# Kernel optimization log

Measured on AMD Instinct MI355X. Metric: run time of the kernel, lower is better.

Reference implementation:

```python
import jax, jax.numpy as jnp
import numpy as np

HIDDEN = 2048
NUM_V = 16
NUM_K = 8
HK = 128
HV = 128
KCONV = 4
KEY_DIM = NUM_K * HK      # 1024
VALUE_DIM = NUM_V * HV    # 2048
CONV_DIM = 2 * KEY_DIM + VALUE_DIM  # 4096
R = NUM_V // NUM_K        # 2
L2_EPS = 1e-6
NORM_EPS = 1e-6


def setup_inputs() -> dict:
    key = jax.random.key(0)
    ks = jax.random.split(key, 8)
    s = 0.02
    return {
        "hidden_states": jax.random.normal(ks[0], (1, 1024, HIDDEN), jnp.float32),
        "w_qkvz": jax.random.normal(ks[1], (2 * KEY_DIM + 2 * VALUE_DIM, HIDDEN), jnp.float32) * s,
        "w_ba": jax.random.normal(ks[2], (2 * NUM_V, HIDDEN), jnp.float32) * s,
        "conv_w": jax.random.normal(ks[3], (CONV_DIM, KCONV), jnp.float32) * s,
        "dt_bias": jnp.ones((NUM_V,), jnp.float32),
        "A_log": jnp.log(jax.random.uniform(ks[4], (NUM_V,), jnp.float32, 1e-3, 16.0)),
        "norm_weight": jnp.ones((HV,), jnp.float32),
        "w_out": jax.random.normal(ks[5], (HIDDEN, VALUE_DIM), jnp.float32) * s,
    }


def reference(hidden_states, w_qkvz, w_ba, conv_w, dt_bias, A_log, norm_weight, w_out):
    B, T, _ = hidden_states.shape
    # --- input projections ---
    qkvz = hidden_states @ w_qkvz.T                     # [B,T,2K+2V]
    ba = hidden_states @ w_ba.T                         # [B,T,2*Hv]
    # fix_query_key_value_ordering: group by k-head, layout [hk, hk, r*hv, r*hv]
    qkvz = qkvz.reshape(B, T, NUM_K, 2 * HK + 2 * R * HV)
    q, k, v, z = jnp.split(qkvz, [HK, 2 * HK, 2 * HK + R * HV], axis=3)
    v = v.reshape(B, T, NUM_V, HV)
    z = z.reshape(B, T, NUM_V, HV)
    ba = ba.reshape(B, T, NUM_K, 2 * R)
    b = ba[..., :R].reshape(B, T, NUM_V)
    a = ba[..., R:].reshape(B, T, NUM_V)
    # --- depthwise causal conv1d + silu over concatenated q,k,v ---
    mixed = jnp.concatenate(
        [q.reshape(B, T, KEY_DIM), k.reshape(B, T, KEY_DIM), v.reshape(B, T, VALUE_DIM)], axis=-1
    )
    xc = mixed.transpose(0, 2, 1)                       # [B,C,T]
    yc = jax.lax.conv_general_dilated(
        xc, conv_w[:, None, :], (1,), [(KCONV - 1, 0)],
        feature_group_count=CONV_DIM, dimension_numbers=("NCH", "OIH", "NCH"),
    )
    yc = jax.nn.silu(yc).transpose(0, 2, 1)             # [B,T,C]
    q, k, v = jnp.split(yc, [KEY_DIM, 2 * KEY_DIM], axis=-1)
    q = q.reshape(B, T, NUM_K, HK)
    k = k.reshape(B, T, NUM_K, HK)
    v = v.reshape(B, T, NUM_V, HV)
    # --- gates ---
    beta = jax.nn.sigmoid(b)                            # [B,T,Hv]
    g = -jnp.exp(A_log) * jax.nn.softplus(a + dt_bias)  # [B,T,Hv] (log decay, <=0)
    # GQA expansion of q,k to value heads
    q = jnp.repeat(q, R, axis=2)                        # [B,T,Hv,hk]
    k = jnp.repeat(k, R, axis=2)
    # l2 norm on q,k (use_qk_l2norm_in_kernel=True)
    q = q * jax.lax.rsqrt(jnp.sum(q * q, -1, keepdims=True) + L2_EPS)
    k = k * jax.lax.rsqrt(jnp.sum(k * k, -1, keepdims=True) + L2_EPS)
    scale = HK ** -0.5
    # --- gated delta rule recurrence ---
    def step(S, xs):
        qt, kt, vt, gt, bt = xs                          # per-timestep slices
        S = S * jnp.exp(gt)[..., None, None]             # decay state [B,Hv,hk,hv]
        kv = jnp.einsum("bhk,bhkv->bhv", kt, S)          # readout at k_t
        delta = (vt - kv) * bt[..., None]                # beta-gated delta
        S = S + jnp.einsum("bhk,bhv->bhkv", kt, delta)
        o = jnp.einsum("bhk,bhkv->bhv", qt * scale, S)
        return S, o

    S0 = jnp.zeros((B, NUM_V, HK, HV), hidden_states.dtype)
    xs = (
        q.transpose(1, 0, 2, 3), k.transpose(1, 0, 2, 3), v.transpose(1, 0, 2, 3),
        g.transpose(1, 0, 2), beta.transpose(1, 0, 2),
    )
    _, o = jax.lax.scan(step, S0, xs)                   # o: [T,B,Hv,hv]
    o = o.transpose(1, 0, 2, 3)                         # [B,T,Hv,hv]
    # --- gated RMSNorm (gate applied before normalization, Mamba2/Qwen3Next style) ---
    xf = o.astype(jnp.float32) * jax.nn.silu(z.astype(jnp.float32))
    var = jnp.mean(xf * xf, -1, keepdims=True)
    xn = xf * jax.lax.rsqrt(var + NORM_EPS) * norm_weight
    # --- output projection ---
    return xn.reshape(B, T, VALUE_DIM) @ w_out.T
```

## Files before the change

### kernel.cpp

```cpp
#include <hip/hip_runtime.h>
#include <math.h>

#define T_LEN   1024
#define HIDDEN  2048
#define QKVZ_N  6144
#define VAL_DIM 2048

typedef _Float16 half8 __attribute__((ext_vector_type(8)));
typedef _Float16 half4 __attribute__((ext_vector_type(4)));
typedef _Float16 half2t __attribute__((ext_vector_type(2)));
typedef float floatx4 __attribute__((ext_vector_type(4)));

__device__ __forceinline__ float sigmoidf_(float x) { return 1.f / (1.f + expf(-x)); }

__device__ __forceinline__ void gl_lds16(const _Float16* g, _Float16* l) {
    __builtin_amdgcn_global_load_lds(
        (const __attribute__((address_space(1))) void*)g,
        (__attribute__((address_space(3))) void*)l, 16, 0, 0);
}

__global__ __launch_bounds__(256) void cvt3(const float* __restrict__ s0, _Float16* __restrict__ d0, int n0,
                                            const float* __restrict__ s1, _Float16* __restrict__ d1, int n1,
                                            const float* __restrict__ s2, _Float16* __restrict__ d2, int n2) {
    int i = blockIdx.x * 256 + threadIdx.x;
    const float* s;
    _Float16* d;
    if (i < n0) { s = s0; d = d0; }
    else if (i < n0 + n1) { s = s1; d = d1; i -= n0; }
    else if (i < n0 + n1 + n2) { s = s2; d = d2; i -= n0 + n1; }
    else return;
    const float4 v = ((const float4*)s)[i];
    half4 h;
    h[0] = (_Float16)v.x; h[1] = (_Float16)v.y;
    h[2] = (_Float16)v.z; h[3] = (_Float16)v.w;
    *(half4*)&d[i * 4] = h;
}

template <int NT, typename OutT>
__global__ __launch_bounds__(256, 2) void gemm_h16(const _Float16* __restrict__ A,
                                                   const _Float16* __restrict__ W,
                                                   OutT* __restrict__ C,
                                                   int MB, int NB, int K) {
    const int BN = NT * 32;
    const int N = NB * BN;
    const int l = blockIdx.x;
    const int x = l & 7;
    const int tt = l >> 3;
    const int mb = tt % MB;
    const int nb = x + 8 * (tt / MB);
    const int m0 = mb * 64, n0 = nb * BN;

    const int t = threadIdx.x;
    const int wave = t >> 6;
    const int lane = t & 63;
    const int wr = (wave >> 1) * 32;
    const int wc = (wave & 1) * (BN / 2);
    const int l15 = lane & 15;
    const int quad = lane >> 4;
    const int srow = lane >> 3;
    const int slot = lane & 7;

    __shared__ __align__(16) _Float16 Ah[2][4096];
    __shared__ __align__(16) _Float16 Bh[2][BN * 64];

    floatx4 acc[2][NT];
#pragma unroll
    for (int i = 0; i < 2; ++i)
#pragma unroll
        for (int j = 0; j < NT; ++j) acc[i][j] = 0;

    auto stage = [&](int buf, int k0) {
#pragma unroll
        for (int g = 0; g < 2; ++g) {
            const int r = wave * 16 + g * 8 + srow;
            const int kc = slot ^ (r & 7);
            gl_lds16(A + (size_t)(m0 + r) * K + k0 + kc * 8,
                     &Ah[buf][(wave * 128 + g * 64) * 8]);
        }
#pragma unroll
        for (int g = 0; g < NT; ++g) {
            const int r = wave * (NT * 8) + g * 8 + srow;
            const int kc = slot ^ (r & 7);
            gl_lds16(W + (size_t)(n0 + r) * K + k0 + kc * 8,
                     &Bh[buf][(wave * (NT * 64) + g * 64) * 8]);
        }
    };

    const int NIT = K >> 6;
    stage(0, 0);
    __syncthreads();
    int cur = 0;
    for (int it = 0; it < NIT; ++it) {
        if (it + 1 < NIT) stage(cur ^ 1, (it + 1) * 64);
        half8 af[2][2], bf[NT][2];
#pragma unroll
        for (int mt = 0; mt < 2; ++mt)
#pragma unroll
            for (int ks = 0; ks < 2; ++ks) {
                const int m = wr + mt * 16 + l15;
                const int kq = ks * 4 + quad;
                af[mt][ks] = *(const half8*)&Ah[cur][(m * 8 + (kq ^ (m & 7))) * 8];
            }
#pragma unroll
        for (int nt = 0; nt < NT; ++nt)
#pragma unroll
            for (int ks = 0; ks < 2; ++ks) {
                const int n = wc + nt * 16 + l15;
                const int kq = ks * 4 + quad;
                bf[nt][ks] = *(const half8*)&Bh[cur][(n * 8 + (kq ^ (n & 7))) * 8];
            }
#pragma unroll
        for (int mt = 0; mt < 2; ++mt)
#pragma unroll
            for (int nt = 0; nt < NT; ++nt)
#pragma unroll
                for (int ks = 0; ks < 2; ++ks)
                    acc[mt][nt] = __builtin_amdgcn_mfma_f32_16x16x32_f16(
                        af[mt][ks], bf[nt][ks], acc[mt][nt], 0, 0, 0);
        if (it + 1 < NIT) {
            __syncthreads();
            cur ^= 1;
        }
    }
#pragma unroll
    for (int mt = 0; mt < 2; ++mt)
#pragma unroll
        for (int nt = 0; nt < NT; ++nt) {
            const int c = n0 + wc + nt * 16 + l15;
#pragma unroll
            for (int reg = 0; reg < 4; ++reg) {
                const int r = m0 + wr + mt * 16 + quad * 4 + reg;
                C[(size_t)r * N + c] = (OutT)acc[mt][nt][reg];
            }
        }
}

__global__ __launch_bounds__(256) void gemm_ba_gates(const float* __restrict__ A,
                                                     const float* __restrict__ W,
                                                     const float* __restrict__ dt_bias,
                                                     const float* __restrict__ A_log,
                                                     float* __restrict__ lgd,
                                                     float* __restrict__ bet) {
    const int m = blockIdx.x;
    const int tid = threadIdx.x;
    const int kl = tid & 31;
    const int ng = tid >> 5;
    const float* Arow = A + (size_t)m * 2048;
    __shared__ float sba[32];

    float4 a4[16];
#pragma unroll
    for (int j = 0; j < 16; ++j)
        a4[j] = *(const float4*)(Arow + j * 128 + kl * 4);

#pragma unroll
    for (int nn = 0; nn < 4; ++nn) {
        const int n = nn * 8 + ng;
        const float* Wrow = W + (size_t)n * 2048;
        float acc = 0.f;
#pragma unroll
        for (int j = 0; j < 16; ++j) {
            const float4 w4 = *(const float4*)(Wrow + j * 128 + kl * 4);
            acc = fmaf(a4[j].x, w4.x, acc);
            acc = fmaf(a4[j].y, w4.y, acc);
            acc = fmaf(a4[j].z, w4.z, acc);
            acc = fmaf(a4[j].w, w4.w, acc);
        }
        acc += __shfl_xor(acc, 1, 64);
        acc += __shfl_xor(acc, 2, 64);
        acc += __shfl_xor(acc, 4, 64);
        acc += __shfl_xor(acc, 8, 64);
        acc += __shfl_xor(acc, 16, 64);
        if (kl == 0) sba[n] = acc;
    }
    __syncthreads();
    if (tid < 16) {
        const int vh = tid, kh = vh >> 1, r = vh & 1;
        const float b = sba[kh * 4 + r];
        const float a = sba[kh * 4 + 2 + r];
        bet[m * 16 + vh] = 1.f / (1.f + expf(-b));
        const float xx = a + dt_bias[vh];
        const float sp = (xx > 0.f) ? (xx + log1pf(expf(-xx))) : log1pf(expf(xx));
        lgd[m * 16 + vh] = -expf(A_log[vh]) * sp;
    }
}

__global__ __launch_bounds__(512) void conv_silu_l2(const _Float16* __restrict__ qkvz,
                                                    const float* __restrict__ conv_w,
                                                    _Float16* __restrict__ qc,
                                                    _Float16* __restrict__ kc,
                                                    _Float16* __restrict__ vc) {
    const int t = blockIdx.x;
    const int c = threadIdx.x * 8;
    int col;
    _Float16* dst;
    bool isqk;
    float extra = 1.f;
    if (c < 1024) {
        col = ((c >> 7) * 768) + (c & 127);
        dst = qc + t * 1024 + c;
        isqk = true;
        extra = 0.08838834764831845f;
    } else if (c < 2048) {
        const int cc = c - 1024;
        col = ((cc >> 7) * 768) + 128 + (cc & 127);
        dst = kc + t * 1024 + cc;
        isqk = true;
    } else {
        const int cc = c - 2048;
        col = ((cc >> 8) * 768) + 256 + (cc & 255);
        dst = vc + (size_t)t * 2048 + cc;
        isqk = false;
    }
    const size_t gb = (size_t)t * QKVZ_N + col;
    const half8 x3 = *(const half8*)(qkvz + gb);
    half8 x2, x1, x0;
    if (t >= 1) x2 = *(const half8*)(qkvz + gb - QKVZ_N);
    if (t >= 2) x1 = *(const half8*)(qkvz + gb - 2 * (size_t)QKVZ_N);
    if (t >= 3) x0 = *(const half8*)(qkvz + gb - 3 * (size_t)QKVZ_N);

    float y[8];
    float ss = 0.f;
#pragma unroll
    for (int u = 0; u < 8; ++u) {
        const float4 wv = *(const float4*)(conv_w + (c + u) * 4);
        float acc = (float)x3[u] * wv.w;
        if (t >= 1) acc = fmaf((float)x2[u], wv.z, acc);
        if (t >= 2) acc = fmaf((float)x1[u], wv.y, acc);
        if (t >= 3) acc = fmaf((float)x0[u], wv.x, acc);
        acc = acc * (1.f / (1.f + expf(-acc)));
        y[u] = acc;
        ss = fmaf(acc, acc, ss);
    }
    half8 ov;
    if (isqk) {
        ss += __shfl_xor(ss, 1, 64);
        ss += __shfl_xor(ss, 2, 64);
        ss += __shfl_xor(ss, 4, 64);
        ss += __shfl_xor(ss, 8, 64);
        const float r = rsqrtf(ss + 1e-6f) * extra;
#pragma unroll
        for (int u = 0; u < 8; ++u) ov[u] = (_Float16)(y[u] * r);
    } else {
#pragma unroll
        for (int u = 0; u < 8; ++u) ov[u] = (_Float16)y[u];
    }
    *(half8*)dst = ov;
}

__global__ __launch_bounds__(256, 1) void chunk_prep(
    const _Float16* __restrict__ qch, const _Float16* __restrict__ kch,
    const _Float16* __restrict__ vch, const float* __restrict__ lgd,
    const float* __restrict__ bet, _Float16* __restrict__ CH,
    float* __restrict__ gamC) {
    const int blk = blockIdx.x;
    const int c = blk >> 4, h = blk & 15, kh = h >> 1;
    const int c0 = c * 64;
    const int tid = threadIdx.x, lane = tid & 63, wave = tid >> 6;
    const int l15 = lane & 15, quad = lane >> 4;

    __shared__ __align__(16) _Float16 Ksh[8192];
    __shared__ __align__(16) _Float16 Qsh[8192];
    __shared__ __align__(16) float Amat[64 * 68];
    __shared__ float Gs[64], Bets[64], Gam[64];

#pragma unroll
    for (int i = 0; i < 17; ++i) Amat[tid + i * 256] = 0.f;

    {
        const int t = tid >> 2, kc0 = (tid & 3) * 4;
        const size_t gb = (size_t)(c0 + t) * 1024 + kh * 128;
#pragma unroll
        for (int i = 0; i < 4; ++i) {
            const int kc = kc0 + i;
            half8 kv = *(const half8*)(kch + gb + kc * 8);
            half8 qv = *(const half8*)(qch + gb + kc * 8);
            const int chl = t * 16 + (kc ^ (t & 15));
            *(half8*)&Ksh[chl * 8] = kv;
            *(half8*)&Qsh[chl * 8] = qv;
        }
    }
    if (tid < 64) {
        float g = lgd[(size_t)(c0 + tid) * 16 + h];
#pragma unroll
        for (int off = 1; off < 64; off <<= 1) {
            float y = __shfl_up(g, off, 64);
            if (tid >= off) g += y;
        }
        Gs[tid] = g;
        Gam[tid] = expf(g);
        Bets[tid] = bet[(size_t)(c0 + tid) * 16 + h];
    }
    __syncthreads();

    _Float16* CHb = CH + (size_t)(c * 16 + h) * 36864;
    _Float16* Ug = CHb;
    _Float16* Wtg = CHb + 8192;
    _Float16* Khg = CHb + 16384;
    _Float16* Qgg = CHb + 24576;
    _Float16* Lg = CHb + 32768;

    {
        floatx4 accKK[4], accQK[4];
#pragma unroll
        for (int tt = 0; tt < 4; ++tt) { accKK[tt] = 0; accQK[tt] = 0; }
        half8 bfK[4];
#pragma unroll
        for (int ks = 0; ks < 4; ++ks) {
            const int i = wave * 16 + l15;
            const int kc = ks * 4 + quad;
            bfK[ks] = *(const half8*)&Ksh[(i * 16 + (kc ^ (i & 15))) * 8];
        }
#pragma unroll
        for (int tt = 0; tt < 4; ++tt) {
            const int t = tt * 16 + l15;
#pragma unroll
            for (int ks = 0; ks < 4; ++ks) {
                const int kc = ks * 4 + quad;
                const int chl = (t * 16 + (kc ^ (t & 15))) * 8;
                half8 afK = *(const half8*)&Ksh[chl];
                half8 afQ = *(const half8*)&Qsh[chl];
                accKK[tt] = __builtin_amdgcn_mfma_f32_16x16x32_f16(afK, bfK[ks], accKK[tt], 0, 0, 0);
                accQK[tt] = __builtin_amdgcn_mfma_f32_16x16x32_f16(afQ, bfK[ks], accQK[tt], 0, 0, 0);
            }
        }
        const int ii = wave * 16 + l15;
        const float Gi = Gs[ii];
#pragma unroll
        for (int tt = 0; tt < 4; ++tt)
#pragma unroll
            for (int r = 0; r < 4; ++r) {
                const int t = tt * 16 + quad * 4 + r;
                const float Gt = Gs[t];
                const float ratio = (ii <= t) ? expf(Gt - Gi) : 0.f;
                if (ii < t) Amat[t * 68 + ii] = Bets[t] * ratio * accKK[tt][r];
                Lg[t * 64 + ii] = (_Float16)((ii <= t) ? ratio * accQK[tt][r] : 0.f);
            }
    }
    __syncthreads();

    {
        const int j = tid;
        float x[64];
        if (j < 128) {
#pragma unroll
            for (int t = 0; t < 64; ++t)
                x[t] = Bets[t] * (float)vch[(size_t)(c0 + t) * 2048 + h * 128 + j];
        } else {
            const int k = j - 128;
#pragma unroll
            for (int t = 0; t < 64; ++t) {
                const int chl = t * 16 + ((k >> 3) ^ (t & 15));
                x[t] = Bets[t] * Gam[t] * (float)Ksh[chl * 8 + (k & 7)];
            }
        }
#pragma unroll
        for (int t = 1; t < 64; ++t) {
            const int nq = (t + 3) >> 2;
            float s0 = 0.f, s1 = 0.f, s2 = 0.f, s3 = 0.f;
#pragma unroll
            for (int q = 0; q < nq; ++q) {
                const float4 a = *(const float4*)&Amat[t * 68 + q * 4];
                s0 = fmaf(a.x, x[q * 4 + 0], s0);
                s1 = fmaf(a.y, x[q * 4 + 1], s1);
                s2 = fmaf(a.z, x[q * 4 + 2], s2);
                s3 = fmaf(a.w, x[q * 4 + 3], s3);
            }
            x[t] -= (s0 + s1) + (s2 + s3);
        }
        if (j < 128) {
#pragma unroll
            for (int t = 0; t < 64; t += 4) {
                half4 w4;
                w4[0] = (_Float16)x[t]; w4[1] = (_Float16)x[t + 1];
                w4[2] = (_Float16)x[t + 2]; w4[3] = (_Float16)x[t + 3];
                *(half4*)&Wtg[j * 64 + t] = w4;
            }
        } else {
            const int k = j - 128;
#pragma unroll
            for (int t = 0; t < 64; ++t) Ug[t * 128 + k] = (_Float16)x[t];
        }
    }

    {
        const float g63 = Gs[63];
        const int k = tid >> 1, cb = (tid & 1) * 32;
#pragma unroll
        for (int cc = 0; cc < 32; cc += 4) {
            half4 o4;
#pragma unroll
            for (int u = 0; u < 4; ++u) {
                const int ci = cb + cc + u;
                const int chl = ci * 16 + ((k >> 3) ^ (ci & 15));
                o4[u] = (_Float16)(expf(g63 - Gs[ci]) * (float)Ksh[chl * 8 + (k & 7)]);
            }
            *(half4*)&Khg[k * 64 + cb + cc] = o4;
        }
        const int cq = tid >> 2, kb = (tid & 3) * 4;
        const float gam = Gam[cq];
#pragma unroll
        for (int kc = 0; kc < 4; ++kc) {
            const int kcc = kb + kc;
            half8 q8 = *(const half8*)&Qsh[(cq * 16 + (kcc ^ (cq & 15))) * 8];
            half8 s8;
#pragma unroll
            for (int u = 0; u < 8; ++u) s8[u] = (_Float16)(gam * (float)q8[u]);
            *(half8*)&Qgg[cq * 128 + kcc * 8] = s8;
        }
        if (tid == 0) gamC[c * 16 + h] = Gam[63];
    }
}

struct ScanOps {
    half8 aU[4];
    half8 aQ[4];
    half8 aL[2];
    half8 aK[2][2];
    half4 wv;
    float gC;
};

__global__ __launch_bounds__(256) void chunk_scan(const _Float16* __restrict__ CH,
                                                  const float* __restrict__ gamC,
                                                  float* __restrict__ o) {
    const int h = blockIdx.x & 15;
    const int vsl = blockIdx.x >> 4;
    const int tid = threadIdx.x, lane = tid & 63, wave = tid >> 6;
    const int l15 = lane & 15, quad = lane >> 4;
    const int tw = wave * 16;
    const int kw = wave * 32;
    const int sKey = l15 << 1;
    const int dKey = (l15 << 1) & 14;

    __shared__ __align__(16) _Float16 Ssh[16 * 128];
    __shared__ __align__(16) _Float16 Dsh[16 * 64];

    *(half8*)&Ssh[tid * 8] = half8{0, 0, 0, 0, 0, 0, 0, 0};
    floatx4 Sacc[2];
    Sacc[0] = 0; Sacc[1] = 0;
    __syncthreads();

    auto loadOps = [&](ScanOps& S, int c) {
        const _Float16* CHb = CH + (size_t)(c * 16 + h) * 36864;
#pragma unroll
        for (int ks = 0; ks < 4; ++ks) {
            S.aU[ks] = *(const half8*)(CHb + (tw + l15) * 128 + ks * 32 + quad * 8);
            S.aQ[ks] = *(const half8*)(CHb + 24576 + (tw + l15) * 128 + ks * 32 + quad * 8);
        }
#pragma unroll
        for (int cs = 0; cs < 2; ++cs) {
            S.aL[cs] = *(const half8*)(CHb + 32768 + (tw + l15) * 64 + cs * 32 + quad * 8);
#pragma unroll
            for (int kt = 0; kt < 2; ++kt)
                S.aK[kt][cs] = *(const half8*)(CHb + 16384 + (kw + kt * 16 + l15) * 64 + cs * 32 + quad * 8);
        }
        S.wv = *(const half4*)(CHb + 8192 + (vsl * 16 + l15) * 64 + tw + quad * 4);
        S.gC = gamC[c * 16 + h];
    };

    auto chunkBody = [&](const ScanOps& S, int c) {
        half8 bs[4];
#pragma unroll
        for (int ks = 0; ks < 4; ++ks)
            bs[ks] = *(const half8*)&Ssh[(l15 * 32 + ((ks * 8 + quad * 2) ^ sKey)) * 4];
        floatx4 xa = {0.f, 0.f, 0.f, 0.f};
#pragma unroll
        for (int ks = 0; ks < 4; ++ks)
            xa = __builtin_amdgcn_mfma_f32_16x16x32_f16(S.aU[ks], bs[ks], xa, 0, 0, 0);
        half4 d4;
#pragma unroll
        for (int r = 0; r < 4; ++r) d4[r] = (_Float16)((float)S.wv[r] - xa[r]);
        *(half4*)&Dsh[(l15 * 16 + ((wave * 4 + quad) ^ dKey)) * 4] = d4;
        __syncthreads();

        half8 bd[2];
#pragma unroll
        for (int cs = 0; cs < 2; ++cs)
            bd[cs] = *(const half8*)&Dsh[(l15 * 16 + ((cs * 8 + quad * 2) ^ dKey)) * 4];
        floatx4 oacc = {0.f, 0.f, 0.f, 0.f};
#pragma unroll
        for (int ks = 0; ks < 4; ++ks)
            oacc = __builtin_amdgcn_mfma_f32_16x16x32_f16(S.aQ[ks], bs[ks], oacc, 0, 0, 0);
#pragma unroll
        for (int cs = 0; cs < 2; ++cs)
            oacc = __builtin_amdgcn_mfma_f32_16x16x32_f16(S.aL[cs], bd[cs], oacc, 0, 0, 0);
#pragma unroll
        for (int kt = 0; kt < 2; ++kt) {
#pragma unroll
            for (int r = 0; r < 4; ++r) Sacc[kt][r] *= S.gC;
#pragma unroll
            for (int cs = 0; cs < 2; ++cs)
                Sacc[kt] = __builtin_amdgcn_mfma_f32_16x16x32_f16(S.aK[kt][cs], bd[cs], Sacc[kt], 0, 0, 0);
        }
        const int col = h * 128 + vsl * 16 + l15;
#pragma unroll
        for (int r = 0; r < 4; ++r)
            o[(size_t)(c * 64 + tw + quad * 4 + r) * 2048 + col] = oacc[r];
#pragma unroll
        for (int kt = 0; kt < 2; ++kt) {
            half4 s4;
#pragma unroll
            for (int r = 0; r < 4; ++r) s4[r] = (_Float16)Sacc[kt][r];
            *(half4*)&Ssh[(l15 * 32 + ((wave * 8 + kt * 4 + quad) ^ sKey)) * 4] = s4;
        }
        __syncthreads();
    };

    ScanOps A_, B_;
    loadOps(A_, 0);
#pragma unroll 1
    for (int cc = 0; cc < 16; cc += 2) {
        loadOps(B_, cc + 1);
        chunkBody(A_, cc);
        if (cc + 2 < 16) loadOps(A_, cc + 2);
        chunkBody(B_, cc + 1);
    }
}

__global__ __launch_bounds__(64) void gated_norm(const float* __restrict__ o,
                                                 const _Float16* __restrict__ qkvz,
                                                 const float* __restrict__ nw,
                                                 _Float16* __restrict__ xn) {
    const int b = blockIdx.x;
    const int t = b >> 4;
    const int vh = b & 15;
    const int kh = vh >> 1;
    const int r = vh & 1;
    const float* op = o + (size_t)t * 2048 + vh * 128;
    const _Float16* zp = qkvz + (size_t)t * QKVZ_N + kh * 768 + 512 + r * 128;
    const int j = threadIdx.x * 2;
    const float2 ov = *(const float2*)(op + j);
    const half2t zv = *(const half2t*)(zp + j);
    const float z0 = (float)zv[0], z1 = (float)zv[1];
    const float f0 = ov.x * z0 / (1.f + expf(-z0));
    const float f1 = ov.y * z1 / (1.f + expf(-z1));
    float ss = f0 * f0 + f1 * f1;
#pragma unroll
    for (int m = 1; m < 64; m <<= 1) ss += __shfl_xor(ss, m, 64);
    const float rs = rsqrtf(ss * (1.f / 128.f) + 1e-6f);
    _Float16* xp = xn + (size_t)t * 2048 + vh * 128;
    half2t y;
    y[0] = (_Float16)(f0 * rs * nw[j]);
    y[1] = (_Float16)(f1 * rs * nw[j + 1]);
    *(half2t*)(xp + j) = y;
}

extern "C" void kernel_launch(void* const* d_in, const int* in_sizes, int n_in,
                              void* d_out, int out_size, void* d_ws, size_t ws_size,
                              hipStream_t stream) {
    const float* hidden  = (const float*)d_in[0];
    const float* w_qkvz  = (const float*)d_in[1];
    const float* w_ba    = (const float*)d_in[2];
    const float* conv_w  = (const float*)d_in[3];
    const float* dt_bias = (const float*)d_in[4];
    const float* A_log   = (const float*)d_in[5];
    const float* norm_w  = (const float*)d_in[6];
    const float* w_out   = (const float*)d_in[7];
    float* out = (float*)d_out;

    char* w = (char*)d_ws;
    _Float16*  qkvz_h = (_Float16*)(w);
    _Float16*  qch    = (_Float16*)(w + 12713984);
    _Float16*  kch    = (_Float16*)(w + 14811136);
    _Float16*  vch    = (_Float16*)(w + 16908288);
    float*     lgd    = (float*)(w + 21102592);
    float*     bet    = (float*)(w + 21168128);
    float*     gamC   = (float*)(w + 21233664);
    float*     o      = (float*)(w + 21237760);
    _Float16*  hid_h  = (_Float16*)(w + 21237760);
    _Float16*  wqk_h  = (_Float16*)(w + 29626368);
    _Float16*  CH     = (_Float16*)(w + 29626368);
    _Float16*  xn_h   = (_Float16*)(w + 29626368 + 18874368);
    _Float16*  wout_h = (_Float16*)(w + 54792192);

    const int n0 = HIDDEN * T_LEN / 4;
    const int n1 = QKVZ_N * HIDDEN / 4;
    const int n2 = VAL_DIM * HIDDEN / 4;
    cvt3<<<(n0 + n1 + n2 + 255) / 256, 256, 0, stream>>>(hidden, hid_h, n0,
                                                         w_qkvz, wqk_h, n1,
                                                         w_out, wout_h, n2);

    gemm_h16<4, _Float16><<<16 * 48, 256, 0, stream>>>(hid_h, wqk_h, qkvz_h, 16, 48, HIDDEN);
    gemm_ba_gates<<<T_LEN, 256, 0, stream>>>(hidden, w_ba, dt_bias, A_log, lgd, bet);
    conv_silu_l2<<<T_LEN, 512, 0, stream>>>(qkvz_h, conv_w, qch, kch, vch);
    chunk_prep<<<256, 256, 0, stream>>>(qch, kch, vch, lgd, bet, CH, gamC);
    chunk_scan<<<128, 256, 0, stream>>>(CH, gamC, o);
    gated_norm<<<T_LEN * 16, 64, 0, stream>>>(o, qkvz_h, norm_w, xn_h);
    gemm_h16<2, float><<<16 * 32, 256, 0, stream>>>(xn_h, wout_h, out, 16, 32, HIDDEN);
}
```

Baseline: 277.4 us.

## Fuse hidden-state fp16 cast into gate GEMM and split chunk_prep across two blocks

The fp32-to-fp16 conversion of hidden_states moves out of the standalone cast kernel and into gemm_ba_gates, which already loads each row into registers. That kernel now runs before the main projection GEMM so the fp16 activations are ready in time. chunk_prep is also split into two 128-thread blocks per (chunk, head): one builds W and the decayed K, the other builds U and the scaled Q, and both redundantly compute the KK Gram matrix for their triangular solve. This doubles the block count to improve occupancy and parallelism, at the cost of recomputing the MFMA work and loading K/Q twice.

```diff
diff --git a/kernel.cpp b/kernel.cpp
--- a/kernel.cpp
+++ b/kernel.cpp
@@ -19,15 +19,13 @@
         (__attribute__((address_space(3))) void*)l, 16, 0, 0);
 }
 
-__global__ __launch_bounds__(256) void cvt3(const float* __restrict__ s0, _Float16* __restrict__ d0, int n0,
-                                            const float* __restrict__ s1, _Float16* __restrict__ d1, int n1,
+__global__ __launch_bounds__(256) void cvt2(const float* __restrict__ s1, _Float16* __restrict__ d1, int n1,
                                             const float* __restrict__ s2, _Float16* __restrict__ d2, int n2) {
     int i = blockIdx.x * 256 + threadIdx.x;
     const float* s;
     _Float16* d;
-    if (i < n0) { s = s0; d = d0; }
-    else if (i < n0 + n1) { s = s1; d = d1; i -= n0; }
-    else if (i < n0 + n1 + n2) { s = s2; d = d2; i -= n0 + n1; }
+    if (i < n1) { s = s1; d = d1; }
+    else if (i < n1 + n2) { s = s2; d = d2; i -= n1; }
     else return;
     const float4 v = ((const float4*)s)[i];
     half4 h;
@@ -135,12 +133,13 @@
         }
 }
 
-__global__ __launch_bounds__(256) void gemm_ba_gates(const float* __restrict__ A,
-                                                     const float* __restrict__ W,
-                                                     const float* __restrict__ dt_bias,
-                                                     const float* __restrict__ A_log,
-                                                     float* __restrict__ lgd,
-                                                     float* __restrict__ bet) {
+__global__ __launch_bounds__(256, 2) void gemm_ba_gates(const float* __restrict__ A,
+                                                        const float* __restrict__ W,
+                                                        const float* __restrict__ dt_bias,
+                                                        const float* __restrict__ A_log,
+                                                        float* __restrict__ lgd,
+                                                        float* __restrict__ bet,
+                                                        _Float16* __restrict__ hid_h) {
     const int m = blockIdx.x;
     const int tid = threadIdx.x;
     const int kl = tid & 31;
@@ -152,6 +151,16 @@
 #pragma unroll
     for (int j = 0; j < 16; ++j)
         a4[j] = *(const float4*)(Arow + j * 128 + kl * 4);
+
+    if (ng == 0) {
+#pragma unroll
+        for (int j = 0; j < 16; ++j) {
+            half4 h;
+            h[0] = (_Float16)a4[j].x; h[1] = (_Float16)a4[j].y;
+            h[2] = (_Float16)a4[j].z; h[3] = (_Float16)a4[j].w;
+            *(half4*)&hid_h[(size_t)m * 2048 + j * 128 + kl * 4] = h;
+        }
+    }
 
 #pragma unroll
     for (int nn = 0; nn < 4; ++nn) {
@@ -248,13 +257,14 @@
     *(half8*)dst = ov;
 }
 
-__global__ __launch_bounds__(256, 1) void chunk_prep(
+__global__ __launch_bounds__(128, 1) void chunk_prep(
     const _Float16* __restrict__ qch, const _Float16* __restrict__ kch,
     const _Float16* __restrict__ vch, const float* __restrict__ lgd,
     const float* __restrict__ bet, _Float16* __restrict__ CH,
     float* __restrict__ gamC) {
     const int blk = blockIdx.x;
-    const int c = blk >> 4, h = blk & 15, kh = h >> 1;
+    const int pair = blk >> 1, p = blk & 1;
+    const int c = pair >> 4, h = pair & 15, kh = h >> 1;
     const int c0 = c * 64;
     const int tid = threadIdx.x, lane = tid & 63, wave = tid >> 6;
     const int l15 = lane & 15, quad = lane >> 4;
@@ -265,13 +275,13 @@
     __shared__ float Gs[64], Bets[64], Gam[64];
 
 #pragma unroll
-    for (int i = 0; i < 17; ++i) Amat[tid + i * 256] = 0.f;
+    for (int i = 0; i < 34; ++i) Amat[tid + i * 128] = 0.f;
 
     {
-        const int t = tid >> 2, kc0 = (tid & 3) * 4;
+        const int t = tid >> 1, kc0 = (tid & 1) * 8;
         const size_t gb = (size_t)(c0 + t) * 1024 + kh * 128;
 #pragma unroll
-        for (int i = 0; i < 4; ++i) {
+        for (int i = 0; i < 8; ++i) {
             const int kc = kc0 + i;
             half8 kv = *(const half8*)(kch + gb + kc * 8);
             half8 qv = *(const half8*)(qch + gb + kc * 8);
@@ -301,16 +311,20 @@
     _Float16* Lg = CHb + 32768;
 
     {
-        floatx4 accKK[4], accQK[4];
-#pragma unroll
-        for (int tt = 0; tt < 4; ++tt) { accKK[tt] = 0; accQK[tt] = 0; }
-        half8 bfK[4];
-#pragma unroll
-        for (int ks = 0; ks < 4; ++ks) {
-            const int i = wave * 16 + l15;
-            const int kc = ks * 4 + quad;
-            bfK[ks] = *(const half8*)&Ksh[(i * 16 + (kc ^ (i & 15))) * 8];
-        }
+        floatx4 accKK[2][4], accQK[2][4];
+#pragma unroll
+        for (int s = 0; s < 2; ++s)
+#pragma unroll
+            for (int tt = 0; tt < 4; ++tt) { accKK[s][tt] = 0; accQK[s][tt] = 0; }
+        half8 bfK[2][4];
+#pragma unroll
+        for (int s = 0; s < 2; ++s)
+#pragma unroll
+            for (int ks = 0; ks < 4; ++ks) {
+                const int i = (wave * 2 + s) * 16 + l15;
+                const int kc = ks * 4 + quad;
+                bfK[s][ks] = *(const half8*)&Ksh[(i * 16 + (kc ^ (i & 15))) * 8];
+            }
 #pragma unroll
         for (int tt = 0; tt < 4; ++tt) {
             const int t = tt * 16 + l15;
@@ -320,38 +334,44 @@
                 const int chl = (t * 16 + (kc ^ (t & 15))) * 8;
                 half8 afK = *(const half8*)&Ksh[chl];
                 half8 afQ = *(const half8*)&Qsh[chl];
-                accKK[tt] = __builtin_amdgcn_mfma_f32_16x16x32_f16(afK, bfK[ks], accKK[tt], 0, 0, 0);
-                accQK[tt] = __builtin_amdgcn_mfma_f32_16x16x32_f16(afQ, bfK[ks], accQK[tt], 0, 0, 0);
-            }
-        }
-        const int ii = wave * 16 + l15;
-        const float Gi = Gs[ii];
-#pragma unroll
-        for (int tt = 0; tt < 4; ++tt)
-#pragma unroll
-            for (int r = 0; r < 4; ++r) {
-                const int t = tt * 16 + quad * 4 + r;
-                const float Gt = Gs[t];
-                const float ratio = (ii <= t) ? expf(Gt - Gi) : 0.f;
-                if (ii < t) Amat[t * 68 + ii] = Bets[t] * ratio * accKK[tt][r];
-                Lg[t * 64 + ii] = (_Float16)((ii <= t) ? ratio * accQK[tt][r] : 0.f);
-            }
+#pragma unroll
+                for (int s = 0; s < 2; ++s) {
+                    accKK[s][tt] = __builtin_amdgcn_mfma_f32_16x16x32_f16(afK, bfK[s][ks], accKK[s][tt], 0, 0, 0);
+                    accQK[s][tt] = __builtin_amdgcn_mfma_f32_16x16x32_f16(afQ, bfK[s][ks], accQK[s][tt], 0, 0, 0);
+                }
+            }
+        }
+#pragma unroll
+        for (int s = 0; s < 2; ++s) {
+            const int ii = (wave * 2 + s) * 16 + l15;
+            const float Gi = Gs[ii];
+#pragma unroll
+            for (int tt = 0; tt < 4; ++tt)
+#pragma unroll
+                for (int r = 0; r < 4; ++r) {
+                    const int t = tt * 16 + quad * 4 + r;
+                    const float Gt = Gs[t];
+                    const float ratio = (ii <= t) ? expf(Gt - Gi) : 0.f;
+                    if (ii < t) Amat[t * 68 + ii] = Bets[t] * ratio * accKK[s][tt][r];
+                    if (p == 0)
+                        Lg[t * 64 + ii] = (_Float16)((ii <= t) ? ratio * accQK[s][tt][r] : 0.f);
+                }
+        }
     }
     __syncthreads();
 
     {
         const int j = tid;
         float x[64];
-        if (j < 128) {
+        if (p == 0) {
 #pragma unroll
             for (int t = 0; t < 64; ++t)
                 x[t] = Bets[t] * (float)vch[(size_t)(c0 + t) * 2048 + h * 128 + j];
         } else {
-            const int k = j - 128;
 #pragma unroll
             for (int t = 0; t < 64; ++t) {
-                const int chl = t * 16 + ((k >> 3) ^ (t & 15));
-                x[t] = Bets[t] * Gam[t] * (float)Ksh[chl * 8 + (k & 7)];
+                const int chl = t * 16 + ((j >> 3) ^ (t & 15));
+                x[t] = Bets[t] * Gam[t] * (float)Ksh[chl * 8 + (j & 7)];
             }
         }
 #pragma unroll
@@ -368,7 +388,7 @@
             }
             x[t] -= (s0 + s1) + (s2 + s3);
         }
-        if (j < 128) {
+        if (p == 0) {
 #pragma unroll
             for (int t = 0; t < 64; t += 4) {
                 half4 w4;
@@ -377,30 +397,34 @@
                 *(half4*)&Wtg[j * 64 + t] = w4;
             }
         } else {
-            const int k = j - 128;
-#pragma unroll
-            for (int t = 0; t < 64; ++t) Ug[t * 128 + k] = (_Float16)x[t];
-        }
-    }
-
-    {
+#pragma unroll
+            for (int t = 0; t < 64; ++t) Ug[t * 128 + j] = (_Float16)x[t];
+        }
+    }
+
+    if (p == 0) {
         const float g63 = Gs[63];
-        const int k = tid >> 1, cb = (tid & 1) * 32;
-#pragma unroll
-        for (int cc = 0; cc < 32; cc += 4) {
-            half4 o4;
-#pragma unroll
-            for (int u = 0; u < 4; ++u) {
-                const int ci = cb + cc + u;
-                const int chl = ci * 16 + ((k >> 3) ^ (ci & 15));
-                o4[u] = (_Float16)(expf(g63 - Gs[ci]) * (float)Ksh[chl * 8 + (k & 7)]);
-            }
-            *(half4*)&Khg[k * 64 + cb + cc] = o4;
-        }
-        const int cq = tid >> 2, kb = (tid & 3) * 4;
+        const int k = tid;
+#pragma unroll
+        for (int cb2 = 0; cb2 < 2; ++cb2) {
+            const int cb = cb2 * 32;
+#pragma unroll
+            for (int cc = 0; cc < 32; cc += 4) {
+                half4 o4;
+#pragma unroll
+                for (int u = 0; u < 4; ++u) {
+                    const int ci = cb + cc + u;
+                    const int chl = ci * 16 + ((k >> 3) ^ (ci & 15));
+                    o4[u] = (_Float16)(expf(g63 - Gs[ci]) * (float)Ksh[chl * 8 + (k & 7)]);
+                }
+                *(half4*)&Khg[k * 64 + cb + cc] = o4;
+            }
+        }
+    } else {
+        const int cq = tid >> 1, kb = (tid & 1) * 8;
         const float gam = Gam[cq];
 #pragma unroll
-        for (int kc = 0; kc < 4; ++kc) {
+        for (int kc = 0; kc < 8; ++kc) {
             const int kcc = kb + kc;
             half8 q8 = *(const half8*)&Qsh[(cq * 16 + (kcc ^ (cq & 15))) * 8];
             half8 s8;
@@ -574,17 +598,15 @@
     _Float16*  xn_h   = (_Float16*)(w + 29626368 + 18874368);
     _Float16*  wout_h = (_Float16*)(w + 54792192);
 
-    const int n0 = HIDDEN * T_LEN / 4;
     const int n1 = QKVZ_N * HIDDEN / 4;
     const int n2 = VAL_DIM * HIDDEN / 4;
-    cvt3<<<(n0 + n1 + n2 + 255) / 256, 256, 0, stream>>>(hidden, hid_h, n0,
-                                                         w_qkvz, wqk_h, n1,
-                                                         w_out, wout_h, n2);
-
+    cvt2<<<(n1 + n2 + 255) / 256, 256, 0, stream>>>(w_qkvz, wqk_h, n1,
+                                                    w_out, wout_h, n2);
+    gemm_ba_gates<<<T_LEN, 256, 0, stream>>>(hidden, w_ba, dt_bias, A_log,
+                                             lgd, bet, hid_h);
     gemm_h16<4, _Float16><<<16 * 48, 256, 0, stream>>>(hid_h, wqk_h, qkvz_h, 16, 48, HIDDEN);
-    gemm_ba_gates<<<T_LEN, 256, 0, stream>>>(hidden, w_ba, dt_bias, A_log, lgd, bet);
     conv_silu_l2<<<T_LEN, 512, 0, stream>>>(qkvz_h, conv_w, qch, kch, vch);
-    chunk_prep<<<256, 256, 0, stream>>>(qch, kch, vch, lgd, bet, CH, gamC);
+    chunk_prep<<<512, 128, 0, stream>>>(qch, kch, vch, lgd, bet, CH, gamC);
     chunk_scan<<<128, 256, 0, stream>>>(CH, gamC, o);
     gated_norm<<<T_LEN * 16, 64, 0, stream>>>(o, qkvz_h, norm_w, xn_h);
     gemm_h16<2, float><<<16 * 32, 256, 0, stream>>>(xn_h, wout_h, out, 16, 32, HIDDEN);
```

Result: no change. 281.5 us (+1.5%).
